# Optimization experiments

Measured on AMD Instinct MI355X. Metric: run time of the kernel, lower is better.

## Reference

```python
import jax, jax.numpy as jnp
import numpy as np

HEADS = 4
DIM_HEADS = 32


def setup_inputs() -> dict:
    key = jax.random.key(0)
    ks = jax.random.split(key, 6)
    dim = 128
    hidden = HEADS * DIM_HEADS  # 128
    b, h, w = 4, 64, 64
    s = 0.02
    return {
        "x": jax.random.normal(ks[0], (b, dim, h, w), dtype=jnp.float32),
        "wq": jax.random.normal(ks[1], (hidden, dim), dtype=jnp.float32) * s,
        "wk": jax.random.normal(ks[2], (hidden, dim), dtype=jnp.float32) * s,
        "wv": jax.random.normal(ks[3], (hidden, dim), dtype=jnp.float32) * s,
        "wo": jax.random.normal(ks[4], (dim, hidden), dtype=jnp.float32) * s,
        "bo": jnp.zeros((dim,), dtype=jnp.float32),
    }


def reference(x, wq, wk, wv, wo, bo):
    b, c, h, w = x.shape
    n = h * w
    scale = DIM_HEADS ** (-0.5)
    xt = x.reshape(b, c, n)  # [b, c, n]; 1x1 conv == matmul over channel dim
    # project and split heads: [b, heads, dim_heads, n]
    q = jnp.einsum('oc,bcn->bon', wq, xt).reshape(b, HEADS, DIM_HEADS, n)
    k = jnp.einsum('oc,bcn->bon', wk, xt).reshape(b, HEADS, DIM_HEADS, n)
    v = jnp.einsum('oc,bcn->bon', wv, xt).reshape(b, HEADS, DIM_HEADS, n)
    q = q * scale
    sim = jnp.einsum('bhdi,bhdj->bhij', q, k)  # [b, heads, n, n]
    attn = jax.nn.softmax(sim, axis=-1)
    out = jnp.einsum('bhij,bhdj->bhid', attn, v)  # [b, heads, n, dim_heads]
    # permute to [b, heads, dim_heads, n] then merge heads -> channels
    out = out.transpose(0, 1, 3, 2).reshape(b, HEADS * DIM_HEADS, n)
    out = jnp.einsum('oc,bcn->bon', wo, out) + bo[None, :, None]
    return out.reshape(b, -1, h, w)
```

## Files before the change

### kernel.cpp

```cpp
#include <hip/hip_runtime.h>
#include <cstdint>

typedef __bf16 bf16;
typedef __bf16 bf16x2 __attribute__((ext_vector_type(2)));
typedef __bf16 bf16x4 __attribute__((ext_vector_type(4)));
typedef __bf16 bf16x8 __attribute__((ext_vector_type(8)));
typedef float f32x4 __attribute__((ext_vector_type(4)));

#define MFMA16(a, b, c) __builtin_amdgcn_mfma_f32_16x16x32_bf16(a, b, c, 0, 0, 0)

static constexpr int N = 4096;
static constexpr int CDIM = 128;
static constexpr int NH = 4;
static constexpr int DH = 32;

__device__ __forceinline__ uint32_t pack_bf16_trunc(float a, float b) {
    return __builtin_amdgcn_perm(__builtin_bit_cast(uint32_t, b),
                                 __builtin_bit_cast(uint32_t, a), 0x07060302u);
}

__device__ __forceinline__ bf16 to_bf16_rnd(float f) {
    uint32_t u = __builtin_bit_cast(uint32_t, f);
    return __builtin_bit_cast(bf16, (uint16_t)((u + 0x8000u) >> 16));
}

__global__ __launch_bounds__(256) void cvt_w(const float* __restrict__ wq,
                                             const float* __restrict__ wk,
                                             const float* __restrict__ wv,
                                             const float* __restrict__ wo,
                                             bf16* __restrict__ W) {
    int i = blockIdx.x * 256 + threadIdx.x;
    const float qs = 0.17677669529663687f * 1.4426950408889634f;
    W[i]         = (bf16)(wq[i] * qs);
    W[16384 + i] = to_bf16_rnd(wk[i]);
    W[32768 + i] = to_bf16_rnd(wv[i]);
    W[49152 + i] = to_bf16_rnd(wo[i]);
}

__global__ __launch_bounds__(256) void proj_qkv(const float* __restrict__ x,
                                                const bf16* __restrict__ W,
                                                bf16* __restrict__ Q,
                                                bf16* __restrict__ K,
                                                bf16* __restrict__ V) {
    const int b = blockIdx.y;
    const int wt = blockIdx.z;
    const int n0 = blockIdx.x * 64;
    __shared__ __align__(16) bf16 xT[64][136];
    const int tid = threadIdx.x;
    const float* xb = x + (size_t)b * CDIM * N;
    for (int i = tid; i < 64 * 128; i += 256) {
        int n = i & 63, cc = i >> 6;
        xT[n][cc] = to_bf16_rnd(xb[(size_t)cc * N + n0 + n]);
    }
    __syncthreads();

    const int lane = tid & 63, w = tid >> 6;
    const int cr = lane & 15, quad = lane >> 4;

    const bf16* Wm = W + wt * 16384;
    for (int nt = 0; nt < 4; ++nt) {
        bf16x8 bfr[4];
#pragma unroll
        for (int ks = 0; ks < 4; ++ks)
            bfr[ks] = *(const bf16x8*)&xT[nt * 16 + cr][ks * 32 + quad * 8];
#pragma unroll
        for (int ot2 = 0; ot2 < 2; ++ot2) {
            int ot = w * 2 + ot2;
            f32x4 acc = {0.f, 0.f, 0.f, 0.f};
#pragma unroll
            for (int ks = 0; ks < 4; ++ks) {
                bf16x8 afr = *(const bf16x8*)&Wm[(ot * 16 + cr) * 128 + ks * 32 + quad * 8];
                acc = MFMA16(afr, bfr[ks], acc);
            }
            int n = n0 + nt * 16 + cr;
            int o0 = ot * 16 + quad * 4;
            if (wt < 2) {
                bf16* dst = (wt == 0) ? Q : K;
                int h = o0 >> 5, d0 = o0 & 31;
                bf16* p = dst + (((size_t)(b * NH + h) * N + n) * DH + d0);
                *(bf16x2*)p       = (bf16x2){(bf16)acc[0], (bf16)acc[1]};
                *(bf16x2*)(p + 2) = (bf16x2){(bf16)acc[2], (bf16)acc[3]};
            } else {
                int h = o0 >> 5, d0 = o0 & 31;
                int k6 = nt * 16 + cr;
                bf16* p = V + ((size_t)(b * NH + h) * 64 + blockIdx.x) * 2048 + k6;
#pragma unroll
                for (int r = 0; r < 4; ++r)
                    p[(d0 + r) * 64] = (bf16)acc[r];
            }
        }
    }
}

__global__ __launch_bounds__(256, 2) void flash(const bf16* __restrict__ Q,
                                                const bf16* __restrict__ K,
                                                const bf16* __restrict__ V,
                                                bf16* __restrict__ O) {
    const int gid = blockIdx.x;
    const int bh = gid & 15;
    const int tid = threadIdx.x;
    const int w = tid >> 6, lane = tid & 63;
    const int cr = lane & 15, quad = lane >> 4;
    const int q0w = (gid >> 4) * 128 + w * 32;

    __shared__ __align__(16) bf16 Kl[2][64 * 40];
    __shared__ __align__(16) bf16 Vl[2][32 * 72];
    __shared__ __align__(16) bf16 Pb[4][2][16 * 72];

    const bf16* Qb = Q + (size_t)bh * N * DH;
    const bf16* Kb = K + (size_t)bh * N * DH;
    const bf16* Vt = V + (size_t)bh * 64 * 2048;

    const int k_dst = (tid >> 2) * 40 + (tid & 3) * 8;
    const int v_dst = (tid >> 3) * 72 + (tid & 7) * 8;

    bf16x8 qf[2];
#pragma unroll
    for (int g = 0; g < 2; ++g)
        qf[g] = *(const bf16x8*)&Qb[(q0w + g * 16 + cr) * DH + quad * 8];

    bf16x8 ones;
#pragma unroll
    for (int i = 0; i < 8; ++i) ones[i] = (bf16)1.0f;

    f32x4 acc00 = {0,0,0,0}, acc01 = {0,0,0,0};
    f32x4 acc10 = {0,0,0,0}, acc11 = {0,0,0,0};
    f32x4 accL0 = {0,0,0,0}, accL1 = {0,0,0,0};

    {
        bf16x8 kreg = *(const bf16x8*)(Kb + tid * 8);
        bf16x8 vreg = *(const bf16x8*)(Vt + tid * 8);
        *(bf16x8*)&Kl[0][k_dst] = kreg;
        *(bf16x8*)&Vl[0][v_dst] = vreg;
    }
    __syncthreads();

    for (int kt = 0; kt < 64; ++kt) {
        const int cb = kt & 1;
        bf16x8 kreg, vreg;
        if (kt < 63) {
            kreg = *(const bf16x8*)(Kb + (kt + 1) * 2048 + tid * 8);
            vreg = *(const bf16x8*)(Vt + (kt + 1) * 2048 + tid * 8);
        }
        const bf16* Kc = &Kl[cb][0];
        const bf16* Vc = &Vl[cb][0];
        bf16* myP0 = &Pb[w][0][cr * 72];
        bf16* myP1 = &Pb[w][1][cr * 72];

#pragma unroll
        for (int kg = 0; kg < 4; ++kg) {
            bf16x8 ak = *(const bf16x8*)&Kc[(kg * 16 + cr) * 40 + quad * 8];
            f32x4 z = {0,0,0,0};
            f32x4 s0 = MFMA16(ak, qf[0], z);
            f32x4 s1 = MFMA16(ak, qf[1], z);

            uint32_t a0 = pack_bf16_trunc(__builtin_amdgcn_exp2f(s0[0]),
                                          __builtin_amdgcn_exp2f(s0[1]));
            uint32_t a1 = pack_bf16_trunc(__builtin_amdgcn_exp2f(s0[2]),
                                          __builtin_amdgcn_exp2f(s0[3]));
            uint32_t b0 = pack_bf16_trunc(__builtin_amdgcn_exp2f(s1[0]),
                                          __builtin_amdgcn_exp2f(s1[1]));
            uint32_t b1 = pack_bf16_trunc(__builtin_amdgcn_exp2f(s1[2]),
                                          __builtin_amdgcn_exp2f(s1[3]));

            *(bf16x4*)(myP0 + kg * 16 + quad * 4) =
                __builtin_bit_cast(bf16x4, (uint64_t)a0 | ((uint64_t)a1 << 32));
            *(bf16x4*)(myP1 + kg * 16 + quad * 4) =
                __builtin_bit_cast(bf16x4, (uint64_t)b0 | ((uint64_t)b1 << 32));
        }

#pragma unroll
        for (int kv = 0; kv < 2; ++kv) {
            bf16x8 pf0 = *(const bf16x8*)(myP0 + kv * 32 + quad * 8);
            bf16x8 pf1 = *(const bf16x8*)(myP1 + kv * 32 + quad * 8);
            bf16x8 av0 = *(const bf16x8*)&Vc[cr * 72 + kv * 32 + quad * 8];
            bf16x8 av1 = *(const bf16x8*)&Vc[(16 + cr) * 72 + kv * 32 + quad * 8];
            acc00 = MFMA16(av0, pf0, acc00);
            acc01 = MFMA16(av1, pf0, acc01);
            acc10 = MFMA16(av0, pf1, acc10);
            acc11 = MFMA16(av1, pf1, acc11);
            accL0 = MFMA16(ones, pf0, accL0);
            accL1 = MFMA16(ones, pf1, accL1);
        }

        if (kt < 63) {
            *(bf16x8*)&Kl[1 - cb][k_dst] = kreg;
            *(bf16x8*)&Vl[1 - cb][v_dst] = vreg;
        }
        __syncthreads();
    }

    const int b = bh >> 2, h = bh & 3;
    const int d0 = quad * 4;
#pragma unroll
    for (int g = 0; g < 2; ++g) {
        f32x4 a0 = g ? acc10 : acc00;
        f32x4 a1 = g ? acc11 : acc01;
        float l = g ? accL1[0] : accL0[0];
        float inv = __builtin_amdgcn_rcpf(l);
        bf16* Ob = O + ((size_t)b * N + q0w + g * 16 + cr) * CDIM + h * DH;
        *(bf16x2*)(Ob + d0)      = (bf16x2){(bf16)(a0[0] * inv), (bf16)(a0[1] * inv)};
        *(bf16x2*)(Ob + d0 + 2)  = (bf16x2){(bf16)(a0[2] * inv), (bf16)(a0[3] * inv)};
        *(bf16x2*)(Ob + 16 + d0) = (bf16x2){(bf16)(a1[0] * inv), (bf16)(a1[1] * inv)};
        *(bf16x2*)(Ob + 18 + d0) = (bf16x2){(bf16)(a1[2] * inv), (bf16)(a1[3] * inv)};
    }
}

__global__ __launch_bounds__(256) void proj_o(const bf16* __restrict__ A,
                                              const bf16* __restrict__ W,
                                              const float* __restrict__ bo,
                                              float* __restrict__ out) {
    const int b = blockIdx.y;
    const int n0 = blockIdx.x * 64;
    __shared__ __align__(16) bf16 aT[64][136];
    const int tid = threadIdx.x;
    const bf16* Ab = A + (size_t)b * N * CDIM;
    for (int i = tid; i < 64 * 64; i += 256) {
        int c2 = i & 63, n = i >> 6;
        *(uint32_t*)&aT[n][c2 * 2] = *(const uint32_t*)&Ab[(size_t)(n0 + n) * CDIM + c2 * 2];
    }
    __syncthreads();

    const int lane = tid & 63, w = tid >> 6;
    const int cr = lane & 15, quad = lane >> 4;
    const bf16* Wm = W + 3 * 16384;
    const int ot = blockIdx.z * 4 + w;

    for (int nt = 0; nt < 4; ++nt) {
        bf16x8 bfr[4];
#pragma unroll
        for (int ks = 0; ks < 4; ++ks)
            bfr[ks] = *(const bf16x8*)&aT[nt * 16 + cr][ks * 32 + quad * 8];
        f32x4 acc = {0.f, 0.f, 0.f, 0.f};
#pragma unroll
        for (int ks = 0; ks < 4; ++ks) {
            bf16x8 afr = *(const bf16x8*)&Wm[(ot * 16 + cr) * 128 + ks * 32 + quad * 8];
            acc = MFMA16(afr, bfr[ks], acc);
        }
        int n = n0 + nt * 16 + cr;
        int o0 = ot * 16 + quad * 4;
#pragma unroll
        for (int r = 0; r < 4; ++r)
            out[((size_t)b * CDIM + o0 + r) * N + n] = acc[r] + bo[o0 + r];
    }
}

extern "C" void kernel_launch(void* const* d_in, const int* in_sizes, int n_in,
                              void* d_out, int out_size, void* d_ws, size_t ws_size,
                              hipStream_t stream) {
    const float* x  = (const float*)d_in[0];
    const float* wq = (const float*)d_in[1];
    const float* wk = (const float*)d_in[2];
    const float* wv = (const float*)d_in[3];
    const float* wo = (const float*)d_in[4];
    const float* bo = (const float*)d_in[5];

    char* ws = (char*)d_ws;
    bf16* Q = (bf16*)(ws);
    bf16* K = (bf16*)(ws + ((size_t)4 << 20));
    bf16* V = (bf16*)(ws + ((size_t)8 << 20));
    bf16* A = (bf16*)(ws + ((size_t)12 << 20));
    bf16* W = (bf16*)(ws + ((size_t)16 << 20));

    cvt_w<<<64, 256, 0, stream>>>(wq, wk, wv, wo, W);
    proj_qkv<<<dim3(64, 4, 3), 256, 0, stream>>>(x, W, Q, K, V);
    flash<<<512, 256, 0, stream>>>(Q, K, V, A);
    proj_o<<<dim3(64, 4, 2), 256, 0, stream>>>(A, W, bo, (float*)d_out);
}
```

Measured before the change: 153.1 us.

## Switch flash attention to 32x32 MFMA with register-resident P

Rewrites the flash kernel's inner loop to use 32x32x16 bf16 MFMA instructions in place of 16x16x32 ones. The exponentiated score tile now feeds directly from registers as the B operand of the PV MFMA, and the per-wave LDS staging buffer for P is removed. To make the register layout of the score output line up with the PV operand, the V projection kernel writes keys in a permuted order within each 16-key group. This cuts LDS traffic and sync pressure, but depends on the accumulator lane mapping matching the permuted V layout exactly.

```diff
diff --git a/kernel.cpp b/kernel.cpp
--- a/kernel.cpp
+++ b/kernel.cpp
@@ -6,8 +6,10 @@
 typedef __bf16 bf16x4 __attribute__((ext_vector_type(4)));
 typedef __bf16 bf16x8 __attribute__((ext_vector_type(8)));
 typedef float f32x4 __attribute__((ext_vector_type(4)));
+typedef float f32x16 __attribute__((ext_vector_type(16)));
 
 #define MFMA16(a, b, c) __builtin_amdgcn_mfma_f32_16x16x32_bf16(a, b, c, 0, 0, 0)
+#define MFMA32(a, b, c) __builtin_amdgcn_mfma_f32_32x32x16_bf16(a, b, c, 0, 0, 0)
 
 static constexpr int N = 4096;
 static constexpr int CDIM = 128;
@@ -83,7 +85,10 @@
             } else {
                 int h = o0 >> 5, d0 = o0 & 31;
                 int k6 = nt * 16 + cr;
-                bf16* p = V + ((size_t)(b * NH + h) * 64 + blockIdx.x) * 2048 + k6;
+                int r4 = (k6 >> 2) & 3;
+                int slotgrp = ((r4 & 1) << 1) | (r4 >> 1);
+                int kperm = (k6 & ~15) | (slotgrp * 4 + (k6 & 3));
+                bf16* p = V + ((size_t)(b * NH + h) * 64 + blockIdx.x) * 2048 + kperm;
 #pragma unroll
                 for (int r = 0; r < 4; ++r)
                     p[(d0 + r) * 64] = (bf16)acc[r];
@@ -100,12 +105,11 @@
     const int bh = gid & 15;
     const int tid = threadIdx.x;
     const int w = tid >> 6, lane = tid & 63;
-    const int cr = lane & 15, quad = lane >> 4;
+    const int l31 = lane & 31, h = lane >> 5;
     const int q0w = (gid >> 4) * 128 + w * 32;
 
     __shared__ __align__(16) bf16 Kl[2][64 * 40];
     __shared__ __align__(16) bf16 Vl[2][32 * 72];
-    __shared__ __align__(16) bf16 Pb[4][2][16 * 72];
 
     const bf16* Qb = Q + (size_t)bh * N * DH;
     const bf16* Kb = K + (size_t)bh * N * DH;
@@ -114,18 +118,15 @@
     const int k_dst = (tid >> 2) * 40 + (tid & 3) * 8;
     const int v_dst = (tid >> 3) * 72 + (tid & 7) * 8;
 
-    bf16x8 qf[2];
-#pragma unroll
-    for (int g = 0; g < 2; ++g)
-        qf[g] = *(const bf16x8*)&Qb[(q0w + g * 16 + cr) * DH + quad * 8];
+    const bf16x8 qf0 = *(const bf16x8*)&Qb[(q0w + l31) * DH + h * 8];
+    const bf16x8 qf1 = *(const bf16x8*)&Qb[(q0w + l31) * DH + 16 + h * 8];
 
     bf16x8 ones;
 #pragma unroll
     for (int i = 0; i < 8; ++i) ones[i] = (bf16)1.0f;
 
-    f32x4 acc00 = {0,0,0,0}, acc01 = {0,0,0,0};
-    f32x4 acc10 = {0,0,0,0}, acc11 = {0,0,0,0};
-    f32x4 accL0 = {0,0,0,0}, accL1 = {0,0,0,0};
+    f32x16 out = {};
+    f32x16 accL = {};
 
     {
         bf16x8 kreg = *(const bf16x8*)(Kb + tid * 8);
@@ -144,43 +145,46 @@
         }
         const bf16* Kc = &Kl[cb][0];
         const bf16* Vc = &Vl[cb][0];
-        bf16* myP0 = &Pb[w][0][cr * 72];
-        bf16* myP1 = &Pb[w][1][cr * 72];
-
-#pragma unroll
-        for (int kg = 0; kg < 4; ++kg) {
-            bf16x8 ak = *(const bf16x8*)&Kc[(kg * 16 + cr) * 40 + quad * 8];
-            f32x4 z = {0,0,0,0};
-            f32x4 s0 = MFMA16(ak, qf[0], z);
-            f32x4 s1 = MFMA16(ak, qf[1], z);
-
-            uint32_t a0 = pack_bf16_trunc(__builtin_amdgcn_exp2f(s0[0]),
-                                          __builtin_amdgcn_exp2f(s0[1]));
-            uint32_t a1 = pack_bf16_trunc(__builtin_amdgcn_exp2f(s0[2]),
-                                          __builtin_amdgcn_exp2f(s0[3]));
-            uint32_t b0 = pack_bf16_trunc(__builtin_amdgcn_exp2f(s1[0]),
-                                          __builtin_amdgcn_exp2f(s1[1]));
-            uint32_t b1 = pack_bf16_trunc(__builtin_amdgcn_exp2f(s1[2]),
-                                          __builtin_amdgcn_exp2f(s1[3]));
-
-            *(bf16x4*)(myP0 + kg * 16 + quad * 4) =
-                __builtin_bit_cast(bf16x4, (uint64_t)a0 | ((uint64_t)a1 << 32));
-            *(bf16x4*)(myP1 + kg * 16 + quad * 4) =
-                __builtin_bit_cast(bf16x4, (uint64_t)b0 | ((uint64_t)b1 << 32));
-        }
-
-#pragma unroll
-        for (int kv = 0; kv < 2; ++kv) {
-            bf16x8 pf0 = *(const bf16x8*)(myP0 + kv * 32 + quad * 8);
-            bf16x8 pf1 = *(const bf16x8*)(myP1 + kv * 32 + quad * 8);
-            bf16x8 av0 = *(const bf16x8*)&Vc[cr * 72 + kv * 32 + quad * 8];
-            bf16x8 av1 = *(const bf16x8*)&Vc[(16 + cr) * 72 + kv * 32 + quad * 8];
-            acc00 = MFMA16(av0, pf0, acc00);
-            acc01 = MFMA16(av1, pf0, acc01);
-            acc10 = MFMA16(av0, pf1, acc10);
-            acc11 = MFMA16(av1, pf1, acc11);
-            accL0 = MFMA16(ones, pf0, accL0);
-            accL1 = MFMA16(ones, pf1, accL1);
+
+#pragma unroll
+        for (int g2 = 0; g2 < 2; ++g2) {
+            bf16x8 kf0 = *(const bf16x8*)&Kc[(g2 * 32 + l31) * 40 + h * 8];
+            bf16x8 kf1 = *(const bf16x8*)&Kc[(g2 * 32 + l31) * 40 + 16 + h * 8];
+            f32x16 sc = {};
+            sc = MFMA32(kf0, qf0, sc);
+            sc = MFMA32(kf1, qf1, sc);
+
+            uint32_t c0 = pack_bf16_trunc(__builtin_amdgcn_exp2f(sc[0]),
+                                          __builtin_amdgcn_exp2f(sc[1]));
+            uint32_t c1 = pack_bf16_trunc(__builtin_amdgcn_exp2f(sc[2]),
+                                          __builtin_amdgcn_exp2f(sc[3]));
+            uint32_t c2 = pack_bf16_trunc(__builtin_amdgcn_exp2f(sc[4]),
+                                          __builtin_amdgcn_exp2f(sc[5]));
+            uint32_t c3 = pack_bf16_trunc(__builtin_amdgcn_exp2f(sc[6]),
+                                          __builtin_amdgcn_exp2f(sc[7]));
+            uint32_t c4 = pack_bf16_trunc(__builtin_amdgcn_exp2f(sc[8]),
+                                          __builtin_amdgcn_exp2f(sc[9]));
+            uint32_t c5 = pack_bf16_trunc(__builtin_amdgcn_exp2f(sc[10]),
+                                          __builtin_amdgcn_exp2f(sc[11]));
+            uint32_t c6 = pack_bf16_trunc(__builtin_amdgcn_exp2f(sc[12]),
+                                          __builtin_amdgcn_exp2f(sc[13]));
+            uint32_t c7 = pack_bf16_trunc(__builtin_amdgcn_exp2f(sc[14]),
+                                          __builtin_amdgcn_exp2f(sc[15]));
+
+            bf16x8 pB0, pB1;
+            {
+                uint32_t t0[4] = {c0, c1, c2, c3};
+                uint32_t t1[4] = {c4, c5, c6, c7};
+                pB0 = *(bf16x8*)t0;
+                pB1 = *(bf16x8*)t1;
+            }
+
+            bf16x8 av0 = *(const bf16x8*)&Vc[l31 * 72 + g2 * 32 + h * 8];
+            bf16x8 av1 = *(const bf16x8*)&Vc[l31 * 72 + g2 * 32 + 16 + h * 8];
+            out = MFMA32(av0, pB0, out);
+            out = MFMA32(av1, pB1, out);
+            accL = MFMA32(ones, pB0, accL);
+            accL = MFMA32(ones, pB1, accL);
         }
 
         if (kt < 63) {
@@ -190,19 +194,15 @@
         __syncthreads();
     }
 
-    const int b = bh >> 2, h = bh & 3;
-    const int d0 = quad * 4;
-#pragma unroll
-    for (int g = 0; g < 2; ++g) {
-        f32x4 a0 = g ? acc10 : acc00;
-        f32x4 a1 = g ? acc11 : acc01;
-        float l = g ? accL1[0] : accL0[0];
-        float inv = __builtin_amdgcn_rcpf(l);
-        bf16* Ob = O + ((size_t)b * N + q0w + g * 16 + cr) * CDIM + h * DH;
-        *(bf16x2*)(Ob + d0)      = (bf16x2){(bf16)(a0[0] * inv), (bf16)(a0[1] * inv)};
-        *(bf16x2*)(Ob + d0 + 2)  = (bf16x2){(bf16)(a0[2] * inv), (bf16)(a0[3] * inv)};
-        *(bf16x2*)(Ob + 16 + d0) = (bf16x2){(bf16)(a1[0] * inv), (bf16)(a1[1] * inv)};
-        *(bf16x2*)(Ob + 18 + d0) = (bf16x2){(bf16)(a1[2] * inv), (bf16)(a1[3] * inv)};
+    const float inv = __builtin_amdgcn_rcpf(accL[0]);
+    const int b = bh >> 2, hh = bh & 3;
+    bf16* Ob = O + ((size_t)b * N + q0w + l31) * CDIM + hh * DH;
+#pragma unroll
+    for (int rg = 0; rg < 4; ++rg) {
+        const int d0 = rg * 8 + h * 4;
+        bf16x4 v = {(bf16)(out[rg * 4 + 0] * inv), (bf16)(out[rg * 4 + 1] * inv),
+                    (bf16)(out[rg * 4 + 2] * inv), (bf16)(out[rg * 4 + 3] * inv)};
+        *(bf16x4*)(Ob + d0) = v;
     }
 }
 
```

New measurement: 136.4 us. -10.9%, faster.
